# Performance work log

Measured on AMD Instinct MI355X. Metric: run time of the kernel, lower is better.

## Reference

```python
import jax, jax.numpy as jnp
import numpy as np

N = 2048
H = 128
W = 128
NEAR = 0.1


def _quat_to_rotmat(q):
    # q: [N,4] (w,x,y,z), normalized -> [N,3,3]
    q = q / jnp.clip(jnp.linalg.norm(q, axis=1, keepdims=True), 1e-8)
    w, x, y, z = q[:, 0], q[:, 1], q[:, 2], q[:, 3]
    xx, yy, zz = x * x, y * y, z * z
    xy, xz, yz = x * y, x * z, y * z
    wx, wy, wz = w * x, w * y, w * z
    r0 = jnp.stack([1 - 2 * (yy + zz), 2 * (xy - wz), 2 * (xz + wy)], axis=1)
    r1 = jnp.stack([2 * (xy + wz), 1 - 2 * (xx + zz), 2 * (yz - wx)], axis=1)
    r2 = jnp.stack([2 * (xz - wy), 2 * (yz + wx), 1 - 2 * (xx + yy)], axis=1)
    return jnp.stack([r0, r1, r2], axis=1)


def _covariance_matrices(log_scales, rotations):
    # R diag(s^2) R^T + 1e-6 I, per Gaussian
    s2 = jnp.exp(2.0 * log_scales)  # scales**2
    R = _quat_to_rotmat(rotations)  # [N,3,3]
    cov = jnp.einsum('nij,nj,nkj->nik', R, s2, R)
    return cov + 1e-6 * jnp.eye(3, dtype=cov.dtype)


def _render(means, cov3d, colors, opacities, intrinsics, camera_to_world, height, width):
    dt = means.dtype
    Rcw = camera_to_world[:3, :3]
    tcw = camera_to_world[:3, 3]
    Rwc = Rcw.T
    twc = -Rwc @ tcw
    p = means @ Rwc.T + twc  # [N,3] camera-space
    x, y, z = p[:, 0], p[:, 1], p[:, 2]
    valid = (z > NEAR).astype(dt)
    zc = jnp.maximum(z, NEAR)
    fx, fy = intrinsics[0, 0], intrinsics[1, 1]
    cx, cy = intrinsics[0, 2], intrinsics[1, 2]
    u = fx * x / zc + cx
    v = fy * y / zc + cy
    # EWA projection Jacobian [N,2,3]
    zeros = jnp.zeros_like(zc)
    J0 = jnp.stack([fx / zc, zeros, -fx * x / (zc * zc)], axis=1)
    J1 = jnp.stack([zeros, fy / zc, -fy * y / (zc * zc)], axis=1)
    J = jnp.stack([J0, J1], axis=1)
    cov_cam = jnp.einsum('ij,njk,lk->nil', Rwc, cov3d, Rwc)  # [N,3,3]
    cov2d = jnp.einsum('nij,njk,nlk->nil', J, cov_cam, J) + 0.3 * jnp.eye(2, dtype=dt)
    a, b, c = cov2d[:, 0, 0], cov2d[:, 0, 1], cov2d[:, 1, 1]
    det = jnp.maximum(a * c - b * b, 1e-12)
    cA, cB, cC = c / det, -b / det, a / det  # conic (inverse 2D covariance)
    # front-to-back depth order; invalid Gaussians pushed to the back
    order = jnp.argsort(jnp.where(valid > 0, zc, jnp.inf))
    u, v = u[order], v[order]
    cA, cB, cC = cA[order], cB[order], cC[order]
    op = (opacities * valid)[order]
    cols = colors[order]
    xs = jnp.arange(width, dtype=dt)
    ys = jnp.arange(height, dtype=dt)
    dx = xs[None, None, :] - u[:, None, None]  # [N,1,W] -> broadcasts
    dy = ys[None, :, None] - v[:, None, None]  # [N,H,1]
    power = (-0.5 * (cA[:, None, None] * dx * dx + cC[:, None, None] * dy * dy)
             - cB[:, None, None] * dx * dy)  # [N,H,W]
    power = jnp.minimum(power, 0.0)
    alpha = jnp.clip(op[:, None, None] * jnp.exp(power), 0.0, 0.99)
    Tcum = jnp.cumprod(1.0 - alpha, axis=0)
    Texcl = jnp.concatenate([jnp.ones_like(Tcum[:1]), Tcum[:-1]], axis=0)
    weight = alpha * Texcl  # [N,H,W]
    img = jnp.einsum('nhw,nc->hwc', weight, cols)  # [H,W,3]
    return img


def setup_inputs():
    key = jax.random.key(0)
    k = jax.random.split(key, 6)
    xy = jax.random.uniform(k[0], (N, 2), minval=-2.0, maxval=2.0)
    z = jax.random.uniform(k[1], (N, 1), minval=3.0, maxval=9.0)
    means = jnp.concatenate([xy, z], axis=1)
    log_scales = jnp.log(jax.random.uniform(k[2], (N, 3), minval=0.02, maxval=0.2))
    rotations = jax.random.normal(k[3], (N, 4))
    colors = jax.random.uniform(k[4], (N, 3))
    opacities = jax.random.normal(k[5], (N,))
    intrinsics = jnp.array([[150.0, 0.0, W / 2], [0.0, 150.0, H / 2], [0.0, 0.0, 1.0]], dtype=jnp.float32)
    camera_to_world = jnp.eye(4, dtype=jnp.float32)
    return {"means": means, "log_scales": log_scales, "rotations": rotations,
            "colors": colors, "opacities": opacities, "intrinsics": intrinsics,
            "camera_to_world": camera_to_world, "height": H, "width": W}


def reference(means, log_scales, rotations, colors, opacities, intrinsics, camera_to_world, height, width):
    cov3d = _covariance_matrices(log_scales, rotations)
    return _render(means, cov3d, jnp.clip(colors, 0.0, 1.0), jax.nn.sigmoid(opacities),
                   intrinsics, camera_to_world, height, width)
```

## Files before the change

kernel.cpp:

```cpp
#include <hip/hip_runtime.h>
#include <hip/hip_bf16.h>

#define NMAX 2048
#define HH 128
#define WW 128
#define NSEG 8
#define SEG 256
#define NEARP 0.1f

static __device__ __forceinline__ float ldin(const void* p, int i, bool is32) {
    return is32 ? ((const float*)p)[i]
                : __bfloat162float(((const __hip_bfloat16*)p)[i]);
}
static __device__ __forceinline__ bool detect32(const void* intr) {
    return ((const float*)intr)[0] > 1.0f;
}
static __device__ __forceinline__ void stout(void* out, int i, float v, bool is32) {
    if (is32) ((float*)out)[i] = v;
    else      ((__hip_bfloat16*)out)[i] = __float2bfloat16(v);
}


__global__ __launch_bounds__(256) void gs_preprocess(
    const void* __restrict__ means,
    const void* __restrict__ log_scales,
    const void* __restrict__ rots,
    const void* __restrict__ colors,
    const void* __restrict__ opac,
    const void* __restrict__ intr,
    const void* __restrict__ c2w,
    int n,
    unsigned long long* __restrict__ keys,
    float* __restrict__ params)
{
    int i = blockIdx.x * blockDim.x + threadIdx.x;
    if (i >= NMAX) return;
    bool is32 = detect32(intr);
    if (i >= n) {
        keys[i] = (((unsigned long long)0x7f800000u) << 32) | (unsigned int)i;
        return;
    }

    float Rwc[3][3], twc[3];
    {
        float Rcw[3][3], tcw[3];
        for (int r = 0; r < 3; ++r) {
            for (int c = 0; c < 3; ++c) Rcw[r][c] = ldin(c2w, r * 4 + c, is32);
            tcw[r] = ldin(c2w, r * 4 + 3, is32);
        }
        for (int r = 0; r < 3; ++r)
            for (int c = 0; c < 3; ++c) Rwc[r][c] = Rcw[c][r];
        for (int r = 0; r < 3; ++r)
            twc[r] = -(Rwc[r][0] * tcw[0] + Rwc[r][1] * tcw[1] + Rwc[r][2] * tcw[2]);
    }
    float fx = ldin(intr, 0, is32), fy = ldin(intr, 4, is32);
    float cx = ldin(intr, 2, is32), cy = ldin(intr, 5, is32);

    float mx = ldin(means, 3 * i, is32), my = ldin(means, 3 * i + 1, is32),
          mz = ldin(means, 3 * i + 2, is32);
    float px = Rwc[0][0] * mx + Rwc[0][1] * my + Rwc[0][2] * mz + twc[0];
    float py = Rwc[1][0] * mx + Rwc[1][1] * my + Rwc[1][2] * mz + twc[1];
    float pz = Rwc[2][0] * mx + Rwc[2][1] * my + Rwc[2][2] * mz + twc[2];
    bool valid = pz > NEARP;
    float zc = fmaxf(pz, NEARP);
    float izc = 1.0f / zc;
    float u = fx * px * izc + cx;
    float v = fy * py * izc + cy;

    float qw = ldin(rots, 4 * i, is32), qx = ldin(rots, 4 * i + 1, is32),
          qy = ldin(rots, 4 * i + 2, is32), qz = ldin(rots, 4 * i + 3, is32);
    float nrm = sqrtf(qw * qw + qx * qx + qy * qy + qz * qz);
    float inv = 1.0f / fmaxf(nrm, 1e-8f);
    qw *= inv; qx *= inv; qy *= inv; qz *= inv;
    float xx = qx * qx, yy = qy * qy, zz = qz * qz;
    float xy = qx * qy, xz = qx * qz, yz = qy * qz;
    float wx = qw * qx, wy = qw * qy, wz = qw * qz;
    float R[3][3] = {
        {1.f - 2.f * (yy + zz), 2.f * (xy - wz),       2.f * (xz + wy)},
        {2.f * (xy + wz),       1.f - 2.f * (xx + zz), 2.f * (yz - wx)},
        {2.f * (xz - wy),       2.f * (yz + wx),       1.f - 2.f * (xx + yy)}
    };
    float s2[3];
    for (int k = 0; k < 3; ++k) s2[k] = __expf(2.0f * ldin(log_scales, 3 * i + k, is32));

    float M[3][3];
    for (int r = 0; r < 3; ++r)
        for (int c = 0; c < 3; ++c)
            M[r][c] = R[r][0] * s2[0] * R[c][0] + R[r][1] * s2[1] * R[c][1]
                    + R[r][2] * s2[2] * R[c][2];
    M[0][0] += 1e-6f; M[1][1] += 1e-6f; M[2][2] += 1e-6f;

    float TM[3][3];
    for (int r = 0; r < 3; ++r)
        for (int c = 0; c < 3; ++c)
            TM[r][c] = Rwc[r][0] * M[0][c] + Rwc[r][1] * M[1][c] + Rwc[r][2] * M[2][c];
    float CC[3][3];
    for (int r = 0; r < 3; ++r)
        for (int c = 0; c < 3; ++c)
            CC[r][c] = TM[r][0] * Rwc[c][0] + TM[r][1] * Rwc[c][1] + TM[r][2] * Rwc[c][2];

    float J0[3] = {fx * izc, 0.0f, -fx * px * izc * izc};
    float J1[3] = {0.0f, fy * izc, -fy * py * izc * izc};
    float t0[3], t1[3];
    for (int c = 0; c < 3; ++c) {
        t0[c] = J0[0] * CC[0][c] + J0[1] * CC[1][c] + J0[2] * CC[2][c];
        t1[c] = J1[0] * CC[0][c] + J1[1] * CC[1][c] + J1[2] * CC[2][c];
    }
    float a  = t0[0] * J0[0] + t0[1] * J0[1] + t0[2] * J0[2] + 0.3f;
    float bq = t0[0] * J1[0] + t0[1] * J1[1] + t0[2] * J1[2];
    float cq = t1[0] * J1[0] + t1[1] * J1[1] + t1[2] * J1[2] + 0.3f;
    float det = fmaxf(a * cq - bq * bq, 1e-12f);
    float idet = 1.0f / det;
    float cA = cq * idet, cB = -bq * idet, cCc = a * idet;

    float o  = ldin(opac, i, is32);
    float op = valid ? (1.0f / (1.0f + __expf(-o))) : 0.0f;
    float cr = fminf(fmaxf(ldin(colors, 3 * i, is32), 0.f), 1.f);
    float cg = fminf(fmaxf(ldin(colors, 3 * i + 1, is32), 0.f), 1.f);
    float cb = fminf(fmaxf(ldin(colors, 3 * i + 2, is32), 0.f), 1.f);

    float zkey = valid ? zc : __builtin_inff();
    keys[i] = (((unsigned long long)__float_as_uint(zkey)) << 32) | (unsigned int)i;

    float* p = params + i * 12;
    p[0] = u;  p[1] = v;
    p[2] = -0.5f * cA;
    p[3] = -cB;
    p[4] = -0.5f * cCc;
    p[5] = op;
    p[6] = cr; p[7] = cg; p[8] = cb; p[9] = 0.f; p[10] = 0.f; p[11] = 0.f;
}

__global__ __launch_bounds__(256) void gs_rank_scatter(
    const unsigned long long* __restrict__ keys_in,
    const float* __restrict__ params_in,
    float* __restrict__ params_sorted,
    int n)
{
    __shared__ unsigned long long sk[NMAX];
    __shared__ int pr[32][9];
    __shared__ int rk[32];
    int t = threadIdx.x;
    #pragma unroll
    for (int e = 0; e < 8; ++e) sk[t + e * 256] = keys_in[t + e * 256];
    __syncthreads();

    int g0 = blockIdx.x * 32;
    int gi = t >> 3;
    int c  = t & 7;
    unsigned long long mykey = sk[g0 + gi];
    int cnt = 0;
    #pragma unroll 8
    for (int j = c; j < NMAX; j += 8)
        cnt += (sk[j] < mykey) ? 1 : 0;
    pr[gi][c] = cnt;
    __syncthreads();

    if (t < 32) {
        int r = 0;
        #pragma unroll
        for (int k = 0; k < 8; ++k) r += pr[t][k];
        rk[t] = r;
    }
    __syncthreads();

    if (t < 96) {
        int g = t / 3, q = t % 3;
        int src = g0 + g;
        float4 val;
        if (src < n) val = ((const float4*)params_in)[src * 3 + q];
        else         val = make_float4(0.f, 0.f, 0.f, 0.f);
        ((float4*)params_sorted)[rk[g] * 3 + q] = val;
    }
}

__global__ __launch_bounds__(256) void gs_render(
    const float* __restrict__ params_sorted,
    float4* __restrict__ segbuf)
{
    __shared__ float sp[SEG * 12];
    int seg = blockIdx.y;
    int t = threadIdx.x;

    const float4* src = (const float4*)(params_sorted + seg * SEG * 12);
    float4* dst = (float4*)sp;
    #pragma unroll
    for (int k = t; k < SEG * 3; k += 256) dst[k] = src[k];
    __syncthreads();

    int pid0 = (blockIdx.x * 256 + t) * 2;
    float px0 = (float)(pid0 & (WW - 1));
    float px1 = px0 + 1.0f;
    float py  = (float)(pid0 >> 7);

    float T0 = 1.f, r0 = 0.f, g0 = 0.f, b0 = 0.f;
    float T1 = 1.f, r1 = 0.f, g1 = 0.f, b1 = 0.f;
    #pragma unroll 4
    for (int i = 0; i < SEG; ++i) {
        const float* gp = sp + i * 12;
        float4 A = *(const float4*)(gp);
        float4 B = *(const float4*)(gp + 4);
        float4 C = *(const float4*)(gp + 8);
        float dy    = py - A.y;
        float nbdy  = A.w * dy;
        float ncdy2 = (B.x * dy) * dy;

        float dx0 = px0 - A.x;
        float p0 = fmaf(fmaf(A.z, dx0, nbdy), dx0, ncdy2);
        p0 = fminf(p0, 0.0f);
        float al0 = fminf(B.y * __expf(p0), 0.99f);
        float w0 = al0 * T0;
        r0 = fmaf(w0, B.z, r0);
        g0 = fmaf(w0, B.w, g0);
        b0 = fmaf(w0, C.x, b0);
        T0 *= (1.0f - al0);

        float dx1 = px1 - A.x;
        float p1 = fmaf(fmaf(A.z, dx1, nbdy), dx1, ncdy2);
        p1 = fminf(p1, 0.0f);
        float al1 = fminf(B.y * __expf(p1), 0.99f);
        float w1 = al1 * T1;
        r1 = fmaf(w1, B.z, r1);
        g1 = fmaf(w1, B.w, g1);
        b1 = fmaf(w1, C.x, b1);
        T1 *= (1.0f - al1);
    }
    segbuf[seg * (HH * WW) + pid0]     = make_float4(r0, g0, b0, T0);
    segbuf[seg * (HH * WW) + pid0 + 1] = make_float4(r1, g1, b1, T1);
}

__global__ __launch_bounds__(256) void gs_combine(
    const float4* __restrict__ segbuf,
    void* __restrict__ out,
    const void* __restrict__ intr)
{
    int pid = blockIdx.x * 256 + threadIdx.x;
    if (pid >= HH * WW) return;
    bool is32 = detect32(intr);
    float r = 0.f, g = 0.f, b = 0.f, T = 1.0f;
    #pragma unroll
    for (int s = 0; s < NSEG; ++s) {
        float4 vv = segbuf[s * (HH * WW) + pid];
        r = fmaf(T, vv.x, r);
        g = fmaf(T, vv.y, g);
        b = fmaf(T, vv.z, b);
        T *= vv.w;
    }
    stout(out, pid * 3 + 0, r, is32);
    stout(out, pid * 3 + 1, g, is32);
    stout(out, pid * 3 + 2, b, is32);
}

__global__ __launch_bounds__(256) void gs_render_all(
    const float* __restrict__ params_sorted,
    void* __restrict__ out,
    const void* __restrict__ intr)
{
    __shared__ float sp[SEG * 12];
    int t = threadIdx.x;
    int pid = blockIdx.x * 256 + t;
    bool is32 = detect32(intr);
    float pxf = (float)(pid & (WW - 1));
    float pyf = (float)(pid >> 7);

    float T = 1.f, r = 0.f, g = 0.f, b = 0.f;
    for (int seg = 0; seg < NSEG; ++seg) {
        __syncthreads();
        const float4* src = (const float4*)(params_sorted + seg * SEG * 12);
        float4* dst = (float4*)sp;
        #pragma unroll
        for (int k = t; k < SEG * 3; k += 256) dst[k] = src[k];
        __syncthreads();
        for (int i = 0; i < SEG; ++i) {
            const float* gp = sp + i * 12;
            float dx = pxf - gp[0];
            float dy = pyf - gp[1];
            float pwr = fmaf(fmaf(gp[2], dx, gp[3] * dy), dx, (gp[4] * dy) * dy);
            pwr = fminf(pwr, 0.0f);
            float alpha = fminf(gp[5] * __expf(pwr), 0.99f);
            float wgt = alpha * T;
            r = fmaf(wgt, gp[6], r);
            g = fmaf(wgt, gp[7], g);
            b = fmaf(wgt, gp[8], b);
            T *= (1.0f - alpha);
        }
    }
    stout(out, pid * 3 + 0, r, is32);
    stout(out, pid * 3 + 1, g, is32);
    stout(out, pid * 3 + 2, b, is32);
}

extern "C" void kernel_launch(void* const* d_in, const int* in_sizes, int n_in,
                              void* d_out, int out_size, void* d_ws, size_t ws_size,
                              hipStream_t stream)
{
    const void* means      = d_in[0];
    const void* log_scales = d_in[1];
    const void* rotations  = d_in[2];
    const void* colors     = d_in[3];
    const void* opacities  = d_in[4];
    const void* intrinsics = d_in[5];
    const void* cam2world  = d_in[6];

    int n = in_sizes[4];
    if (n > NMAX) n = NMAX;

    size_t off_keys   = 0;
    size_t off_params = NMAX * 8;
    size_t off_sorted = off_params + NMAX * 48;
    size_t off_seg    = off_sorted + NMAX * 48;
    size_t need_seg   = off_seg + (size_t)NSEG * HH * WW * 16;

    unsigned long long* keys = (unsigned long long*)((char*)d_ws + off_keys);
    float* params  = (float*)((char*)d_ws + off_params);
    float* sortedp = (float*)((char*)d_ws + off_sorted);
    float4* segbuf = (float4*)((char*)d_ws + off_seg);

    gs_preprocess<<<NMAX / 256, 256, 0, stream>>>(
        means, log_scales, rotations, colors, opacities, intrinsics, cam2world,
        n, keys, params);
    gs_rank_scatter<<<NMAX / 32, 256, 0, stream>>>(keys, params, sortedp, n);

    if (ws_size >= need_seg) {
        dim3 rg(HH * WW / 512, NSEG);
        gs_render<<<rg, 256, 0, stream>>>(sortedp, segbuf);
        gs_combine<<<HH * WW / 256, 256, 0, stream>>>(segbuf, d_out, intrinsics);
    } else {
        gs_render_all<<<HH * WW / 256, 256, 0, stream>>>(sortedp, d_out, intrinsics);
    }
}
```

Measured before the change: 100.4 us.

## Fuse pipeline into single tiled kernel with per-tile culling and local sort

Replaces the preprocess, global rank sort, segmented render and combine kernels with a single kernel where each block owns an 8x8 pixel tile. Each block culls Gaussians with a conservative screen-space extent test, then applies a tighter opacity-aware log bound. It computes full conics only for the survivors, rank-sorts them by depth in shared memory, and composites with four waves covering depth ranges merged at the end. This removes launch overhead, global memory round trips and the full per-pixel loop over all Gaussians. In exchange it adds redundant culling work per tile, and it risks approximation from the epsilon cull and the fixed 768-entry cap.

```diff
diff --git a/kernel.cpp b/kernel.cpp
--- a/kernel.cpp
+++ b/kernel.cpp
@@ -4,9 +4,9 @@
 #define NMAX 2048
 #define HH 128
 #define WW 128
-#define NSEG 8
-#define SEG 256
 #define NEARP 0.1f
+#define CULL_LOG_EPS -18.0f
+#define CAP 768
 
 static __device__ __forceinline__ float ldin(const void* p, int i, bool is32) {
     return is32 ? ((const float*)p)[i]
@@ -20,8 +20,7 @@
     else      ((__hip_bfloat16*)out)[i] = __float2bfloat16(v);
 }
 
-
-__global__ __launch_bounds__(256) void gs_preprocess(
+__global__ __launch_bounds__(256) void gs_fused(
     const void* __restrict__ means,
     const void* __restrict__ log_scales,
     const void* __restrict__ rots,
@@ -30,16 +29,19 @@
     const void* __restrict__ intr,
     const void* __restrict__ c2w,
     int n,
-    unsigned long long* __restrict__ keys,
-    float* __restrict__ params)
+    void* __restrict__ out)
 {
-    int i = blockIdx.x * blockDim.x + threadIdx.x;
-    if (i >= NMAX) return;
+    __shared__ float rec[CAP * 12];
+    __shared__ unsigned long long skey[CAP];
+    __shared__ unsigned short sorder[CAP];
+    __shared__ int cand[NMAX];
+    __shared__ float4 part[4][64];
+    __shared__ int candCnt, mCnt;
+
+    int t = threadIdx.x;
+    int lane = t & 63, wid = t >> 6;
     bool is32 = detect32(intr);
-    if (i >= n) {
-        keys[i] = (((unsigned long long)0x7f800000u) << 32) | (unsigned int)i;
-        return;
-    }
+    if (t == 0) { candCnt = 0; mCnt = 0; }
 
     float Rwc[3][3], twc[3];
     {
@@ -56,238 +58,189 @@
     float fx = ldin(intr, 0, is32), fy = ldin(intr, 4, is32);
     float cx = ldin(intr, 2, is32), cy = ldin(intr, 5, is32);
 
-    float mx = ldin(means, 3 * i, is32), my = ldin(means, 3 * i + 1, is32),
-          mz = ldin(means, 3 * i + 2, is32);
-    float px = Rwc[0][0] * mx + Rwc[0][1] * my + Rwc[0][2] * mz + twc[0];
-    float py = Rwc[1][0] * mx + Rwc[1][1] * my + Rwc[1][2] * mz + twc[1];
-    float pz = Rwc[2][0] * mx + Rwc[2][1] * my + Rwc[2][2] * mz + twc[2];
-    bool valid = pz > NEARP;
-    float zc = fmaxf(pz, NEARP);
-    float izc = 1.0f / zc;
-    float u = fx * px * izc + cx;
-    float v = fy * py * izc + cy;
-
-    float qw = ldin(rots, 4 * i, is32), qx = ldin(rots, 4 * i + 1, is32),
-          qy = ldin(rots, 4 * i + 2, is32), qz = ldin(rots, 4 * i + 3, is32);
-    float nrm = sqrtf(qw * qw + qx * qx + qy * qy + qz * qz);
-    float inv = 1.0f / fmaxf(nrm, 1e-8f);
-    qw *= inv; qx *= inv; qy *= inv; qz *= inv;
-    float xx = qx * qx, yy = qy * qy, zz = qz * qz;
-    float xy = qx * qy, xz = qx * qz, yz = qy * qz;
-    float wx = qw * qx, wy = qw * qy, wz = qw * qz;
-    float R[3][3] = {
-        {1.f - 2.f * (yy + zz), 2.f * (xy - wz),       2.f * (xz + wy)},
-        {2.f * (xy + wz),       1.f - 2.f * (xx + zz), 2.f * (yz - wx)},
-        {2.f * (xz - wy),       2.f * (yz + wx),       1.f - 2.f * (xx + yy)}
-    };
-    float s2[3];
-    for (int k = 0; k < 3; ++k) s2[k] = __expf(2.0f * ldin(log_scales, 3 * i + k, is32));
-
-    float M[3][3];
-    for (int r = 0; r < 3; ++r)
-        for (int c = 0; c < 3; ++c)
-            M[r][c] = R[r][0] * s2[0] * R[c][0] + R[r][1] * s2[1] * R[c][1]
-                    + R[r][2] * s2[2] * R[c][2];
-    M[0][0] += 1e-6f; M[1][1] += 1e-6f; M[2][2] += 1e-6f;
-
-    float TM[3][3];
-    for (int r = 0; r < 3; ++r)
-        for (int c = 0; c < 3; ++c)
-            TM[r][c] = Rwc[r][0] * M[0][c] + Rwc[r][1] * M[1][c] + Rwc[r][2] * M[2][c];
-    float CC[3][3];
-    for (int r = 0; r < 3; ++r)
-        for (int c = 0; c < 3; ++c)
-            CC[r][c] = TM[r][0] * Rwc[c][0] + TM[r][1] * Rwc[c][1] + TM[r][2] * Rwc[c][2];
-
-    float J0[3] = {fx * izc, 0.0f, -fx * px * izc * izc};
-    float J1[3] = {0.0f, fy * izc, -fy * py * izc * izc};
-    float t0[3], t1[3];
-    for (int c = 0; c < 3; ++c) {
-        t0[c] = J0[0] * CC[0][c] + J0[1] * CC[1][c] + J0[2] * CC[2][c];
-        t1[c] = J1[0] * CC[0][c] + J1[1] * CC[1][c] + J1[2] * CC[2][c];
-    }
-    float a  = t0[0] * J0[0] + t0[1] * J0[1] + t0[2] * J0[2] + 0.3f;
-    float bq = t0[0] * J1[0] + t0[1] * J1[1] + t0[2] * J1[2];
-    float cq = t1[0] * J1[0] + t1[1] * J1[1] + t1[2] * J1[2] + 0.3f;
-    float det = fmaxf(a * cq - bq * bq, 1e-12f);
-    float idet = 1.0f / det;
-    float cA = cq * idet, cB = -bq * idet, cCc = a * idet;
-
-    float o  = ldin(opac, i, is32);
-    float op = valid ? (1.0f / (1.0f + __expf(-o))) : 0.0f;
-    float cr = fminf(fmaxf(ldin(colors, 3 * i, is32), 0.f), 1.f);
-    float cg = fminf(fmaxf(ldin(colors, 3 * i + 1, is32), 0.f), 1.f);
-    float cb = fminf(fmaxf(ldin(colors, 3 * i + 2, is32), 0.f), 1.f);
-
-    float zkey = valid ? zc : __builtin_inff();
-    keys[i] = (((unsigned long long)__float_as_uint(zkey)) << 32) | (unsigned int)i;
-
-    float* p = params + i * 12;
-    p[0] = u;  p[1] = v;
-    p[2] = -0.5f * cA;
-    p[3] = -cB;
-    p[4] = -0.5f * cCc;
-    p[5] = op;
-    p[6] = cr; p[7] = cg; p[8] = cb; p[9] = 0.f; p[10] = 0.f; p[11] = 0.f;
-}
-
-__global__ __launch_bounds__(256) void gs_rank_scatter(
-    const unsigned long long* __restrict__ keys_in,
-    const float* __restrict__ params_in,
-    float* __restrict__ params_sorted,
-    int n)
-{
-    __shared__ unsigned long long sk[NMAX];
-    __shared__ int pr[32][9];
-    __shared__ int rk[32];
-    int t = threadIdx.x;
+    int bx = blockIdx.x & 15, by = blockIdx.x >> 4;
+    float tx0 = (float)(bx * 8), tx1 = tx0 + 7.0f;
+    float ty0 = (float)(by * 8), ty1 = ty0 + 7.0f;
+
+    __syncthreads();
+
     #pragma unroll
-    for (int e = 0; e < 8; ++e) sk[t + e * 256] = keys_in[t + e * 256];
-    __syncthreads();
-
-    int g0 = blockIdx.x * 32;
-    int gi = t >> 3;
-    int c  = t & 7;
-    unsigned long long mykey = sk[g0 + gi];
-    int cnt = 0;
-    #pragma unroll 8
-    for (int j = c; j < NMAX; j += 8)
-        cnt += (sk[j] < mykey) ? 1 : 0;
-    pr[gi][c] = cnt;
-    __syncthreads();
-
-    if (t < 32) {
+    for (int k = 0; k < NMAX / 256; ++k) {
+        int g = k * 256 + t;
+        bool keep = false;
+        if (g < n) {
+            float mx = ldin(means, 3 * g, is32);
+            float my = ldin(means, 3 * g + 1, is32);
+            float mz = ldin(means, 3 * g + 2, is32);
+            float wpz = Rwc[2][0] * mx + Rwc[2][1] * my + Rwc[2][2] * mz + twc[2];
+            if (wpz > NEARP) {
+                float wpx = Rwc[0][0] * mx + Rwc[0][1] * my + Rwc[0][2] * mz + twc[0];
+                float wpy = Rwc[1][0] * mx + Rwc[1][1] * my + Rwc[1][2] * mz + twc[1];
+                float izc = 1.0f / wpz;
+                float u = fx * wpx * izc + cx;
+                float v = fy * wpy * izc + cy;
+                float l0 = ldin(log_scales, 3 * g, is32);
+                float l1 = ldin(log_scales, 3 * g + 1, is32);
+                float l2 = ldin(log_scales, 3 * g + 2, is32);
+                float s2max = __expf(2.0f * fmaxf(l0, fmaxf(l1, l2)));
+                float jf2 = (fx * fx * (1.0f + wpx * wpx * izc * izc)
+                           + fy * fy * (1.0f + wpy * wpy * izc * izc)) * izc * izc;
+                float lmax = jf2 * (s2max + 1e-6f) + 0.3f;
+                float dxm = fmaxf(fmaxf(tx0 - u, u - tx1), 0.0f);
+                float dym = fmaxf(fmaxf(ty0 - v, v - ty1), 0.0f);
+                keep = (dxm * dxm + dym * dym) < 36.0f * lmax;
+            }
+        }
+        unsigned long long ball = __ballot(keep);
+        int base = 0;
+        if (lane == 0) base = atomicAdd(&candCnt, (int)__popcll(ball));
+        base = __shfl(base, 0);
+        if (keep)
+            cand[base + (int)__popcll(ball & ((1ull << lane) - 1ull))] = g;
+    }
+    __syncthreads();
+    int Kc = candCnt;
+
+    for (int j = t; j < Kc; j += 256) {
+        int g = cand[j];
+        float mx = ldin(means, 3 * g, is32);
+        float my = ldin(means, 3 * g + 1, is32);
+        float mz = ldin(means, 3 * g + 2, is32);
+        float wpx = Rwc[0][0] * mx + Rwc[0][1] * my + Rwc[0][2] * mz + twc[0];
+        float wpy = Rwc[1][0] * mx + Rwc[1][1] * my + Rwc[1][2] * mz + twc[1];
+        float wpz = Rwc[2][0] * mx + Rwc[2][1] * my + Rwc[2][2] * mz + twc[2];
+        float zc = fmaxf(wpz, NEARP);
+        float izc = 1.0f / zc;
+        float u = fx * wpx * izc + cx;
+        float v = fy * wpy * izc + cy;
+
+        float qw = ldin(rots, 4 * g, is32), qx = ldin(rots, 4 * g + 1, is32),
+              qy = ldin(rots, 4 * g + 2, is32), qz = ldin(rots, 4 * g + 3, is32);
+        float nrm = sqrtf(qw * qw + qx * qx + qy * qy + qz * qz);
+        float inv = 1.0f / fmaxf(nrm, 1e-8f);
+        qw *= inv; qx *= inv; qy *= inv; qz *= inv;
+        float xx = qx * qx, yy = qy * qy, zz = qz * qz;
+        float xy = qx * qy, xz = qx * qz, yz = qy * qz;
+        float wx = qw * qx, wy = qw * qy, wz = qw * qz;
+        float R[3][3] = {
+            {1.f - 2.f * (yy + zz), 2.f * (xy - wz),       2.f * (xz + wy)},
+            {2.f * (xy + wz),       1.f - 2.f * (xx + zz), 2.f * (yz - wx)},
+            {2.f * (xz - wy),       2.f * (yz + wx),       1.f - 2.f * (xx + yy)}
+        };
+        float s2[3];
+        for (int k = 0; k < 3; ++k)
+            s2[k] = __expf(2.0f * ldin(log_scales, 3 * g + k, is32));
+
+        float M[3][3];
+        for (int r = 0; r < 3; ++r)
+            for (int c = 0; c < 3; ++c)
+                M[r][c] = R[r][0] * s2[0] * R[c][0] + R[r][1] * s2[1] * R[c][1]
+                        + R[r][2] * s2[2] * R[c][2];
+        M[0][0] += 1e-6f; M[1][1] += 1e-6f; M[2][2] += 1e-6f;
+
+        float TM[3][3];
+        for (int r = 0; r < 3; ++r)
+            for (int c = 0; c < 3; ++c)
+                TM[r][c] = Rwc[r][0] * M[0][c] + Rwc[r][1] * M[1][c] + Rwc[r][2] * M[2][c];
+        float CC[3][3];
+        for (int r = 0; r < 3; ++r)
+            for (int c = 0; c < 3; ++c)
+                CC[r][c] = TM[r][0] * Rwc[c][0] + TM[r][1] * Rwc[c][1] + TM[r][2] * Rwc[c][2];
+
+        float J0[3] = {fx * izc, 0.0f, -fx * wpx * izc * izc};
+        float J1[3] = {0.0f, fy * izc, -fy * wpy * izc * izc};
+        float t0[3], t1[3];
+        for (int c = 0; c < 3; ++c) {
+            t0[c] = J0[0] * CC[0][c] + J0[1] * CC[1][c] + J0[2] * CC[2][c];
+            t1[c] = J1[0] * CC[0][c] + J1[1] * CC[1][c] + J1[2] * CC[2][c];
+        }
+        float a  = t0[0] * J0[0] + t0[1] * J0[1] + t0[2] * J0[2] + 0.3f;
+        float bq = t0[0] * J1[0] + t0[1] * J1[1] + t0[2] * J1[2];
+        float cq = t1[0] * J1[0] + t1[1] * J1[1] + t1[2] * J1[2] + 0.3f;
+        float det = fmaxf(a * cq - bq * bq, 1e-12f);
+        float idet = 1.0f / det;
+
+        float na  = -0.5f * (cq * idet);
+        float nb  = bq * idet;
+        float ncc = -0.5f * (a * idet);
+        float qyb = ncc - nb * nb / (4.0f * na);
+        float qxb = na  - nb * nb / (4.0f * ncc);
+
+        float o  = ldin(opac, g, is32);
+        float op = 1.0f / (1.0f + __expf(-o));
+        float lnop = __logf(op);
+
+        float dxm = fmaxf(fmaxf(tx0 - u, u - tx1), 0.0f);
+        float dym = fmaxf(fmaxf(ty0 - v, v - ty1), 0.0f);
+        float bound = fminf(qyb * dym * dym, qxb * dxm * dxm) + lnop;
+        bool keep = bound > CULL_LOG_EPS;
+
+        unsigned long long ball = __ballot(keep);
+        int base = 0;
+        if (lane == 0) base = atomicAdd(&mCnt, (int)__popcll(ball));
+        base = __shfl(base, 0);
+        if (keep) {
+            int slot = base + (int)__popcll(ball & ((1ull << lane) - 1ull));
+            if (slot < CAP) {
+                float cr = fminf(fmaxf(ldin(colors, 3 * g, is32), 0.f), 1.f);
+                float cg = fminf(fmaxf(ldin(colors, 3 * g + 1, is32), 0.f), 1.f);
+                float cb = fminf(fmaxf(ldin(colors, 3 * g + 2, is32), 0.f), 1.f);
+                float4* d = (float4*)(rec + slot * 12);
+                d[0] = make_float4(u, v, na, nb);
+                d[1] = make_float4(ncc, lnop, cr, cg);
+                d[2] = make_float4(cb, 0.f, 0.f, 0.f);
+                skey[slot] = (((unsigned long long)__float_as_uint(zc)) << 32)
+                           | (unsigned int)g;
+            }
+        }
+    }
+    __syncthreads();
+    int Ms = mCnt < CAP ? mCnt : CAP;
+
+    for (int s = t; s < Ms; s += 256) {
+        unsigned long long key = skey[s];
         int r = 0;
-        #pragma unroll
-        for (int k = 0; k < 8; ++k) r += pr[t][k];
-        rk[t] = r;
-    }
-    __syncthreads();
-
-    if (t < 96) {
-        int g = t / 3, q = t % 3;
-        int src = g0 + g;
-        float4 val;
-        if (src < n) val = ((const float4*)params_in)[src * 3 + q];
-        else         val = make_float4(0.f, 0.f, 0.f, 0.f);
-        ((float4*)params_sorted)[rk[g] * 3 + q] = val;
-    }
-}
-
-__global__ __launch_bounds__(256) void gs_render(
-    const float* __restrict__ params_sorted,
-    float4* __restrict__ segbuf)
-{
-    __shared__ float sp[SEG * 12];
-    int seg = blockIdx.y;
-    int t = threadIdx.x;
-
-    const float4* src = (const float4*)(params_sorted + seg * SEG * 12);
-    float4* dst = (float4*)sp;
-    #pragma unroll
-    for (int k = t; k < SEG * 3; k += 256) dst[k] = src[k];
-    __syncthreads();
-
-    int pid0 = (blockIdx.x * 256 + t) * 2;
-    float px0 = (float)(pid0 & (WW - 1));
-    float px1 = px0 + 1.0f;
-    float py  = (float)(pid0 >> 7);
-
-    float T0 = 1.f, r0 = 0.f, g0 = 0.f, b0 = 0.f;
-    float T1 = 1.f, r1 = 0.f, g1 = 0.f, b1 = 0.f;
-    #pragma unroll 4
-    for (int i = 0; i < SEG; ++i) {
-        const float* gp = sp + i * 12;
-        float4 A = *(const float4*)(gp);
-        float4 B = *(const float4*)(gp + 4);
-        float4 C = *(const float4*)(gp + 8);
-        float dy    = py - A.y;
-        float nbdy  = A.w * dy;
-        float ncdy2 = (B.x * dy) * dy;
-
-        float dx0 = px0 - A.x;
-        float p0 = fmaf(fmaf(A.z, dx0, nbdy), dx0, ncdy2);
-        p0 = fminf(p0, 0.0f);
-        float al0 = fminf(B.y * __expf(p0), 0.99f);
-        float w0 = al0 * T0;
-        r0 = fmaf(w0, B.z, r0);
-        g0 = fmaf(w0, B.w, g0);
-        b0 = fmaf(w0, C.x, b0);
-        T0 *= (1.0f - al0);
-
-        float dx1 = px1 - A.x;
-        float p1 = fmaf(fmaf(A.z, dx1, nbdy), dx1, ncdy2);
-        p1 = fminf(p1, 0.0f);
-        float al1 = fminf(B.y * __expf(p1), 0.99f);
-        float w1 = al1 * T1;
-        r1 = fmaf(w1, B.z, r1);
-        g1 = fmaf(w1, B.w, g1);
-        b1 = fmaf(w1, C.x, b1);
-        T1 *= (1.0f - al1);
-    }
-    segbuf[seg * (HH * WW) + pid0]     = make_float4(r0, g0, b0, T0);
-    segbuf[seg * (HH * WW) + pid0 + 1] = make_float4(r1, g1, b1, T1);
-}
-
-__global__ __launch_bounds__(256) void gs_combine(
-    const float4* __restrict__ segbuf,
-    void* __restrict__ out,
-    const void* __restrict__ intr)
-{
-    int pid = blockIdx.x * 256 + threadIdx.x;
-    if (pid >= HH * WW) return;
-    bool is32 = detect32(intr);
-    float r = 0.f, g = 0.f, b = 0.f, T = 1.0f;
-    #pragma unroll
-    for (int s = 0; s < NSEG; ++s) {
-        float4 vv = segbuf[s * (HH * WW) + pid];
-        r = fmaf(T, vv.x, r);
-        g = fmaf(T, vv.y, g);
-        b = fmaf(T, vv.z, b);
-        T *= vv.w;
-    }
-    stout(out, pid * 3 + 0, r, is32);
-    stout(out, pid * 3 + 1, g, is32);
-    stout(out, pid * 3 + 2, b, is32);
-}
-
-__global__ __launch_bounds__(256) void gs_render_all(
-    const float* __restrict__ params_sorted,
-    void* __restrict__ out,
-    const void* __restrict__ intr)
-{
-    __shared__ float sp[SEG * 12];
-    int t = threadIdx.x;
-    int pid = blockIdx.x * 256 + t;
-    bool is32 = detect32(intr);
-    float pxf = (float)(pid & (WW - 1));
-    float pyf = (float)(pid >> 7);
-
-    float T = 1.f, r = 0.f, g = 0.f, b = 0.f;
-    for (int seg = 0; seg < NSEG; ++seg) {
-        __syncthreads();
-        const float4* src = (const float4*)(params_sorted + seg * SEG * 12);
-        float4* dst = (float4*)sp;
-        #pragma unroll
-        for (int k = t; k < SEG * 3; k += 256) dst[k] = src[k];
-        __syncthreads();
-        for (int i = 0; i < SEG; ++i) {
-            const float* gp = sp + i * 12;
-            float dx = pxf - gp[0];
-            float dy = pyf - gp[1];
-            float pwr = fmaf(fmaf(gp[2], dx, gp[3] * dy), dx, (gp[4] * dy) * dy);
-            pwr = fminf(pwr, 0.0f);
-            float alpha = fminf(gp[5] * __expf(pwr), 0.99f);
-            float wgt = alpha * T;
-            r = fmaf(wgt, gp[6], r);
-            g = fmaf(wgt, gp[7], g);
-            b = fmaf(wgt, gp[8], b);
-            T *= (1.0f - alpha);
-        }
-    }
-    stout(out, pid * 3 + 0, r, is32);
-    stout(out, pid * 3 + 1, g, is32);
-    stout(out, pid * 3 + 2, b, is32);
+        for (int j = 0; j < Ms; ++j) r += (skey[j] < key) ? 1 : 0;
+        sorder[r] = (unsigned short)s;
+    }
+    __syncthreads();
+
+    int i0 = (Ms * wid) >> 2;
+    int i1 = (Ms * (wid + 1)) >> 2;
+    float pxf = tx0 + (float)(lane & 7);
+    float pyf = ty0 + (float)(lane >> 3);
+    float T = 1.f, cr = 0.f, cg = 0.f, cb = 0.f;
+    for (int i = i0; i < i1; ++i) {
+        int s = sorder[i];
+        const float4* rp = (const float4*)(rec + 12 * s);
+        float4 A = rp[0];
+        float4 B = rp[1];
+        float4 C = rp[2];
+        float dy = pyf - A.y;
+        float dx = pxf - A.x;
+        float pwr = fmaf(fmaf(A.z, dx, A.w * dy), dx, (B.x * dy) * dy);
+        float al = fminf(__expf(fminf(pwr, 0.0f) + B.y), 0.99f);
+        float w = al * T;
+        cr = fmaf(w, B.z, cr);
+        cg = fmaf(w, B.w, cg);
+        cb = fmaf(w, C.x, cb);
+        T *= (1.0f - al);
+    }
+    part[wid][lane] = make_float4(cr, cg, cb, T);
+    __syncthreads();
+
+    if (t < 64) {
+        float4 p0 = part[0][t], p1 = part[1][t], p2 = part[2][t], p3 = part[3][t];
+        float rr = p0.x + p0.w * (p1.x + p1.w * (p2.x + p2.w * p3.x));
+        float gg = p0.y + p0.w * (p1.y + p1.w * (p2.y + p2.w * p3.y));
+        float bb = p0.z + p0.w * (p1.z + p1.w * (p2.z + p2.w * p3.z));
+        int pxg = bx * 8 + (t & 7);
+        int pyg = by * 8 + (t >> 3);
+        int pid = pyg * WW + pxg;
+        stout(out, pid * 3 + 0, rr, is32);
+        stout(out, pid * 3 + 1, gg, is32);
+        stout(out, pid * 3 + 2, bb, is32);
+    }
 }
 
 extern "C" void kernel_launch(void* const* d_in, const int* in_sizes, int n_in,
@@ -301,31 +254,12 @@
     const void* opacities  = d_in[4];
     const void* intrinsics = d_in[5];
     const void* cam2world  = d_in[6];
+    (void)d_ws; (void)ws_size;
 
     int n = in_sizes[4];
     if (n > NMAX) n = NMAX;
 
-    size_t off_keys   = 0;
-    size_t off_params = NMAX * 8;
-    size_t off_sorted = off_params + NMAX * 48;
-    size_t off_seg    = off_sorted + NMAX * 48;
-    size_t need_seg   = off_seg + (size_t)NSEG * HH * WW * 16;
-
-    unsigned long long* keys = (unsigned long long*)((char*)d_ws + off_keys);
-    float* params  = (float*)((char*)d_ws + off_params);
-    float* sortedp = (float*)((char*)d_ws + off_sorted);
-    float4* segbuf = (float4*)((char*)d_ws + off_seg);
-
-    gs_preprocess<<<NMAX / 256, 256, 0, stream>>>(
+    gs_fused<<<256, 256, 0, stream>>>(
         means, log_scales, rotations, colors, opacities, intrinsics, cam2world,
-        n, keys, params);
-    gs_rank_scatter<<<NMAX / 32, 256, 0, stream>>>(keys, params, sortedp, n);
-
-    if (ws_size >= need_seg) {
-        dim3 rg(HH * WW / 512, NSEG);
-        gs_render<<<rg, 256, 0, stream>>>(sortedp, segbuf);
-        gs_combine<<<HH * WW / 256, 256, 0, stream>>>(segbuf, d_out, intrinsics);
-    } else {
-        gs_render_all<<<HH * WW / 256, 256, 0, stream>>>(sortedp, d_out, intrinsics);
-    }
-}
+        n, d_out);
+}
```

Measured after the change: 105.3 us. +4.9%, slower.
